# Kernel tuning notes

Hardware: AMD Instinct MI355X
Metric: run time of the kernel (lower is better)

Reference implementation:

```python
import jax, jax.numpy as jnp
import numpy as np

THRESH = 0.2  # contact probability threshold from _make_graph default


def setup_inputs() -> dict:
    key = jax.random.key(0)
    ks = jax.random.split(key, 10)
    L, D, K, M = 1024, 640, 32, 64
    S = jax.random.normal(ks[0], (L, D), jnp.float32)
    P = jax.random.uniform(ks[1], (L, L), jnp.float32)
    P = 0.5 * (P + P.T)  # symmetric base-pair probability matrix
    xyz = jax.random.normal(ks[2], (L, 3), jnp.float32) * 10.0  # Angstrom-scale C1' coords
    rbf_mu = jnp.linspace(0.0, 30.0, K).astype(jnp.float32)     # RBF centers over 0-30 A
    rbf_sigma = jax.random.uniform(ks[3], (K,), jnp.float32, 0.5, 2.0)
    W_edge = jax.random.normal(ks[4], (K + 2, M), jnp.float32) * 0.05
    b_edge = jnp.zeros((M,), jnp.float32)
    W_node = jax.random.normal(ks[5], (D, M), jnp.float32) * 0.05
    w_out = jax.random.normal(ks[6], (M,), jnp.float32) * 0.1
    return {"S": S, "P": P, "xyz": xyz, "rbf_mu": rbf_mu, "rbf_sigma": rbf_sigma,
            "W_edge": W_edge, "b_edge": b_edge, "W_node": W_node, "w_out": w_out}


def reference(S, P, xyz, rbf_mu, rbf_sigma, W_edge, b_edge, W_node, w_out):
    """Graph construction (_make_graph) + one SE3-style gated coordinate update.

    Edges: backbone (j == i+1, etype=0, pij=1) and high-prob contacts
    (P[i,j] > THRESH, j > i+2, etype=1, pij=P[i,j]). Edge scalars are
    [etype, pij, rbf(d)] exactly as in _make_graph; edge vectors are
    xyz[j]-xyz[i]. Computed in dense masked form for jit-compatibility.
    """
    L = xyz.shape[0]
    rel = xyz[None, :, :] - xyz[:, None, :]                      # (L,L,3) xyz[j]-xyz[i]
    # safe norm: eps avoids nan grad on zero diagonal (diagonal is masked out anyway)
    d = jnp.sqrt(jnp.sum(rel * rel, axis=-1, keepdims=True) + 1e-12)  # (L,L,1)
    rbf_feat = jnp.exp(-(d - rbf_mu) ** 2 / (2.0 * rbf_sigma ** 2))   # (L,L,K)

    idx = jnp.arange(L)
    backbone = idx[None, :] == idx[:, None] + 1                  # j == i+1
    contact = (P > THRESH) & (idx[None, :] > idx[:, None] + 2)   # skip j <= i+2
    mask = backbone | contact                                    # (L,L)

    etype = contact.astype(S.dtype)                              # 0 backbone, 1 contact
    pij = jnp.where(backbone, jnp.asarray(1.0, S.dtype), P)
    e_scalar = jnp.concatenate([etype[..., None], pij[..., None], rbf_feat], axis=-1)  # (L,L,K+2)

    # gather-compute: message from edge scalars + destination-node scalars
    node_proj = S @ W_node                                       # (L,M)
    msg = jax.nn.relu(jnp.einsum('ijk,km->ijm', e_scalar, W_edge) + b_edge
                      + node_proj[None, :, :])                   # (L,L,M)
    gate = jax.nn.sigmoid(msg @ w_out) * mask.astype(S.dtype)    # (L,L)

    # scatter: equivariant coordinate update, sum of gated edge vectors per node
    xyz_out = xyz + jnp.einsum('ij,ijc->ic', gate, rel)          # (L,3)
    return xyz_out
```

## Files before the change

kernel.cpp:

```cpp
#include <hip/hip_runtime.h>
#include <math.h>

#define LL 1024
#define DD 640
#define KK 32
#define MM 64
#define THRESH 0.2f

#define NPROJ_OFF 0
#define WRT_OFF   (LL * MM)
#define W0_OFF    (WRT_OFF + 1024)
#define W1_OFF    (W0_OFF + MM)
#define MU_OFF    (W1_OFF + MM)
#define NIS2_OFF  (MU_OFF + KK)

typedef float f32x4_t __attribute__((ext_vector_type(4)));
typedef short bf16x8_t __attribute__((ext_vector_type(8)));

union FragU { unsigned int u[4]; bf16x8_t v; };

__device__ __forceinline__ unsigned int pack_bf(float hi, float lo) {
    return __builtin_amdgcn_perm(__float_as_uint(hi), __float_as_uint(lo), 0x07060302u);
}

__global__ __launch_bounds__(256) void prep_kernel(
    const float* __restrict__ S, const float* __restrict__ rbf_mu,
    const float* __restrict__ rbf_sigma, const float* __restrict__ W_edge,
    const float* __restrict__ b_edge, const float* __restrict__ W_node,
    float* __restrict__ ws)
{
    __shared__ float red[4][2][64];
    const int b = blockIdx.x;
    const int t = threadIdx.x;
    if (b < LL / 2) {
        const int m = t & 63;
        const int c = t >> 6;
        const int r0 = b * 2;
        float a0 = 0.f, a1 = 0.f;
        const int d0 = c * 160;
        #pragma unroll 2
        for (int dd = d0; dd < d0 + 160; dd += 4) {
            const float4 s0 = *(const float4*)(S + (size_t)r0 * DD + dd);
            const float4 s1 = *(const float4*)(S + (size_t)(r0 + 1) * DD + dd);
            const float w0 = W_node[(dd + 0) * MM + m];
            const float w1 = W_node[(dd + 1) * MM + m];
            const float w2 = W_node[(dd + 2) * MM + m];
            const float w3 = W_node[(dd + 3) * MM + m];
            a0 = fmaf(s0.x, w0, a0); a0 = fmaf(s0.y, w1, a0);
            a0 = fmaf(s0.z, w2, a0); a0 = fmaf(s0.w, w3, a0);
            a1 = fmaf(s1.x, w0, a1); a1 = fmaf(s1.y, w1, a1);
            a1 = fmaf(s1.z, w2, a1); a1 = fmaf(s1.w, w3, a1);
        }
        red[c][0][m] = a0;
        red[c][1][m] = a1;
        __syncthreads();
        if (t < 64) {
            const float be = b_edge[t];
            const float v0 = ((red[0][0][t] + red[1][0][t]) + (red[2][0][t] + red[3][0][t])) + be;
            const float v1 = ((red[0][1][t] + red[1][1][t]) + (red[2][1][t] + red[3][1][t])) + be;
            ws[NPROJ_OFF + (size_t)r0 * MM + t]       = v0;
            ws[NPROJ_OFF + (size_t)(r0 + 1) * MM + t] = v1;
        }
    } else {
        unsigned short* wrt = (unsigned short*)(ws + WRT_OFF);
        if (t < MM) {
            ws[W0_OFF + t] = W_edge[t];
            ws[W1_OFF + t] = W_edge[MM + t];
        }
        if (t < KK) {
            ws[MU_OFF + t] = rbf_mu[t];
            const float s = rbf_sigma[t];
            ws[NIS2_OFF + t] = -1.0f / (2.0f * s * s);
        }
        for (int idx = t; idx < KK * MM; idx += 256) {
            const int m = idx >> 5, k = idx & 31;
            unsigned int u = __float_as_uint(W_edge[(2 + k) * MM + m]);
            u = (u + 0x7fffu + ((u >> 16) & 1u)) >> 16;
            wrt[idx] = (unsigned short)u;
        }
    }
}

__global__ __launch_bounds__(256, 2) void edge_kernel(
    const float* __restrict__ P, const float* __restrict__ xyz,
    const float* __restrict__ w_out, const float* __restrict__ ws,
    float* __restrict__ out)
{
    const int tid  = threadIdx.x;
    const int lane = tid & 63;
    const int wave = tid >> 6;
    const int quad = lane >> 4;
    const int col  = lane & 15;
    __shared__ float sred[4][3];

    const float* __restrict__ nproj = ws + NPROJ_OFF;
    const unsigned short* __restrict__ wrt = (const unsigned short*)(ws + WRT_OFF);

    FragU ar[4], a2[4];
    float wv[4][4];
    float muj[8], nis2[8];
    #pragma unroll
    for (int mt = 0; mt < 4; ++mt) {
        const uint4 w = *(const uint4*)(wrt + (mt * 16 + col) * KK + quad * 8);
        ar[mt].u[0] = w.x; ar[mt].u[1] = w.y; ar[mt].u[2] = w.z; ar[mt].u[3] = w.w;
        const float w0 = ws[W0_OFF + mt * 16 + col];
        const float w1 = ws[W1_OFF + mt * 16 + col];
        a2[mt].u[0] = (quad == 0) ? pack_bf(w1, w0) : 0u;
        a2[mt].u[1] = 0u; a2[mt].u[2] = 0u; a2[mt].u[3] = 0u;
        const float4 wo = *(const float4*)(w_out + mt * 16 + quad * 4);
        wv[mt][0] = wo.x; wv[mt][1] = wo.y; wv[mt][2] = wo.z; wv[mt][3] = wo.w;
    }
    #pragma unroll
    for (int j = 0; j < 8; ++j) {
        muj[j]  = ws[MU_OFF + quad * 8 + j];
        nis2[j] = ws[NIS2_OFF + quad * 8 + j];
    }

    int rows[2];
    rows[0] = (int)blockIdx.x;
    rows[1] = (LL - 1) - (int)blockIdx.x;

    for (int rr = 0; rr < 2; ++rr) {
        const int i = rows[rr];
        const float xi0 = xyz[i * 3 + 0];
        const float xi1 = xyz[i * 3 + 1];
        const float xi2 = xyz[i * 3 + 2];
        float ax = 0.f, ay = 0.f, az = 0.f;
        const int len = (LL - 1) - i;

        for (int base = wave * 64; base < len; base += 256) {
            const int jo = base + lane;
            const bool valid = jo < len;
            const int jc = valid ? (i + 1 + jo) : (LL - 1);
            const float p_own = P[(size_t)i * LL + jc];
            const float rx = xyz[jc * 3 + 0] - xi0;
            const float ry = xyz[jc * 3 + 1] - xi1;
            const float rz = xyz[jc * 3 + 2] - xi2;
            const float d_own = sqrtf(fmaf(rx, rx, fmaf(ry, ry, fmaf(rz, rz, 1e-12f))));
            const bool msk = valid && ((jo == 0) || ((jo >= 2) && (p_own > THRESH)));

            float res[4];
            #pragma unroll
            for (int ct = 0; ct < 4; ++ct) {
                const int src = ct * 16 + col;
                const float d_t = __shfl(d_own, src, 64);
                const float p_t = __shfl(p_own, src, 64);
                const int jo_t = base + src;
                const float et = ((jo_t >= 2) && (p_t > THRESH)) ? 1.0f : 0.0f;
                const float pj = (jo_t == 0) ? 1.0f : p_t;

                float r[8];
                #pragma unroll
                for (int j = 0; j < 8; ++j) {
                    const float t0 = d_t - muj[j];
                    r[j] = __expf(t0 * t0 * nis2[j]);
                }
                FragU bf;
                bf.u[0] = pack_bf(r[1], r[0]); bf.u[1] = pack_bf(r[3], r[2]);
                bf.u[2] = pack_bf(r[5], r[4]); bf.u[3] = pack_bf(r[7], r[6]);
                FragU b2;
                b2.u[0] = (quad == 0) ? pack_bf(pj, et) : 0u;
                b2.u[1] = 0u; b2.u[2] = 0u; b2.u[3] = 0u;

                const int jc_t = (jo_t < len) ? (i + 1 + jo_t) : (LL - 1);
                const float* npr = nproj + (size_t)jc_t * MM;

                float g = 0.0f;
                #pragma unroll
                for (int mt = 0; mt < 4; ++mt) {
                    f32x4_t c0 = *(const f32x4_t*)(npr + mt * 16 + quad * 4);
                    c0 = __builtin_amdgcn_mfma_f32_16x16x32_bf16(ar[mt].v, bf.v, c0, 0, 0, 0);
                    c0 = __builtin_amdgcn_mfma_f32_16x16x32_bf16(a2[mt].v, b2.v, c0, 0, 0, 0);
                    g = fmaf(fmaxf(c0[0], 0.f), wv[mt][0], g);
                    g = fmaf(fmaxf(c0[1], 0.f), wv[mt][1], g);
                    g = fmaf(fmaxf(c0[2], 0.f), wv[mt][2], g);
                    g = fmaf(fmaxf(c0[3], 0.f), wv[mt][3], g);
                }
                g += __shfl_xor(g, 16, 64);
                g += __shfl_xor(g, 32, 64);
                res[ct] = g;
            }
            float gd = res[0];
            gd = (quad == 1) ? res[1] : gd;
            gd = (quad == 2) ? res[2] : gd;
            gd = (quad == 3) ? res[3] : gd;
            const float gate = msk ? (1.0f / (1.0f + __expf(-gd))) : 0.0f;
            ax = fmaf(gate, rx, ax);
            ay = fmaf(gate, ry, ay);
            az = fmaf(gate, rz, az);
        }

        #pragma unroll
        for (int off = 32; off > 0; off >>= 1) {
            ax += __shfl_down(ax, off, 64);
            ay += __shfl_down(ay, off, 64);
            az += __shfl_down(az, off, 64);
        }
        if (lane == 0) {
            sred[wave][0] = ax; sred[wave][1] = ay; sred[wave][2] = az;
        }
        __syncthreads();
        if (tid == 0) {
            const float tx = (sred[0][0] + sred[1][0]) + (sred[2][0] + sred[3][0]);
            const float ty = (sred[0][1] + sred[1][1]) + (sred[2][1] + sred[3][1]);
            const float tz = (sred[0][2] + sred[1][2]) + (sred[2][2] + sred[3][2]);
            out[i * 3 + 0] = xi0 + tx;
            out[i * 3 + 1] = xi1 + ty;
            out[i * 3 + 2] = xi2 + tz;
        }
        __syncthreads();
    }
}

extern "C" void kernel_launch(void* const* d_in, const int* in_sizes, int n_in,
                              void* d_out, int out_size, void* d_ws, size_t ws_size,
                              hipStream_t stream) {
    const float* S         = (const float*)d_in[0];
    const float* P         = (const float*)d_in[1];
    const float* xyz       = (const float*)d_in[2];
    const float* rbf_mu    = (const float*)d_in[3];
    const float* rbf_sigma = (const float*)d_in[4];
    const float* W_edge    = (const float*)d_in[5];
    const float* b_edge    = (const float*)d_in[6];
    const float* W_node    = (const float*)d_in[7];
    const float* w_out     = (const float*)d_in[8];
    float* out = (float*)d_out;
    float* ws  = (float*)d_ws;

    prep_kernel<<<LL / 2 + 1, 256, 0, stream>>>(S, rbf_mu, rbf_sigma, W_edge,
                                                b_edge, W_node, ws);
    edge_kernel<<<LL / 2, 256, 0, stream>>>(P, xyz, w_out, ws, out);
}
```

Measured before the change: 104.2 us.

## Drop second MFMA for etype/pij, recompute per-column distances, widen edge blocks

Replaces the second bf16 MFMA that added the etype/pij edge-scalar contribution with two fp32 FMAs per accumulator element, folded into the node-projection accumulator before the main MFMA. Instead of shuffling distance and P across lanes, each lane reloads P and xyz for its column and recomputes the distance directly. The edge kernel now runs 512-thread blocks (8 waves) with launch bounds (512,4), and the prep loop unroll rises to 4. These aim to cut MFMA count and shuffle traffic and to raise parallelism per row, at the cost of redundant global loads and sqrt work and more register pressure under the tighter launch bound.

```diff
diff --git a/kernel.cpp b/kernel.cpp
--- a/kernel.cpp
+++ b/kernel.cpp
@@ -38,7 +38,7 @@
         const int r0 = b * 2;
         float a0 = 0.f, a1 = 0.f;
         const int d0 = c * 160;
-        #pragma unroll 2
+        #pragma unroll 4
         for (int dd = d0; dd < d0 + 160; dd += 4) {
             const float4 s0 = *(const float4*)(S + (size_t)r0 * DD + dd);
             const float4 s1 = *(const float4*)(S + (size_t)(r0 + 1) * DD + dd);
@@ -81,7 +81,7 @@
     }
 }
 
-__global__ __launch_bounds__(256, 2) void edge_kernel(
+__global__ __launch_bounds__(512, 4) void edge_kernel(
     const float* __restrict__ P, const float* __restrict__ xyz,
     const float* __restrict__ w_out, const float* __restrict__ ws,
     float* __restrict__ out)
@@ -91,24 +91,21 @@
     const int wave = tid >> 6;
     const int quad = lane >> 4;
     const int col  = lane & 15;
-    __shared__ float sred[4][3];
+    __shared__ float sred[8][3];
 
     const float* __restrict__ nproj = ws + NPROJ_OFF;
     const unsigned short* __restrict__ wrt = (const unsigned short*)(ws + WRT_OFF);
 
-    FragU ar[4], a2[4];
-    float wv[4][4];
+    FragU ar[4];
+    f32x4_t w0q[4], w1q[4], wv[4];
     float muj[8], nis2[8];
     #pragma unroll
     for (int mt = 0; mt < 4; ++mt) {
         const uint4 w = *(const uint4*)(wrt + (mt * 16 + col) * KK + quad * 8);
         ar[mt].u[0] = w.x; ar[mt].u[1] = w.y; ar[mt].u[2] = w.z; ar[mt].u[3] = w.w;
-        const float w0 = ws[W0_OFF + mt * 16 + col];
-        const float w1 = ws[W1_OFF + mt * 16 + col];
-        a2[mt].u[0] = (quad == 0) ? pack_bf(w1, w0) : 0u;
-        a2[mt].u[1] = 0u; a2[mt].u[2] = 0u; a2[mt].u[3] = 0u;
-        const float4 wo = *(const float4*)(w_out + mt * 16 + quad * 4);
-        wv[mt][0] = wo.x; wv[mt][1] = wo.y; wv[mt][2] = wo.z; wv[mt][3] = wo.w;
+        w0q[mt] = *(const f32x4_t*)(ws + W0_OFF + mt * 16 + quad * 4);
+        w1q[mt] = *(const f32x4_t*)(ws + W1_OFF + mt * 16 + quad * 4);
+        wv[mt]  = *(const f32x4_t*)(w_out + mt * 16 + quad * 4);
     }
     #pragma unroll
     for (int j = 0; j < 8; ++j) {
@@ -128,7 +125,7 @@
         float ax = 0.f, ay = 0.f, az = 0.f;
         const int len = (LL - 1) - i;
 
-        for (int base = wave * 64; base < len; base += 256) {
+        for (int base = wave * 64; base < len; base += 512) {
             const int jo = base + lane;
             const bool valid = jo < len;
             const int jc = valid ? (i + 1 + jo) : (LL - 1);
@@ -136,41 +133,41 @@
             const float rx = xyz[jc * 3 + 0] - xi0;
             const float ry = xyz[jc * 3 + 1] - xi1;
             const float rz = xyz[jc * 3 + 2] - xi2;
-            const float d_own = sqrtf(fmaf(rx, rx, fmaf(ry, ry, fmaf(rz, rz, 1e-12f))));
             const bool msk = valid && ((jo == 0) || ((jo >= 2) && (p_own > THRESH)));
 
             float res[4];
             #pragma unroll
             for (int ct = 0; ct < 4; ++ct) {
-                const int src = ct * 16 + col;
-                const float d_t = __shfl(d_own, src, 64);
-                const float p_t = __shfl(p_own, src, 64);
-                const int jo_t = base + src;
-                const float et = ((jo_t >= 2) && (p_t > THRESH)) ? 1.0f : 0.0f;
-                const float pj = (jo_t == 0) ? 1.0f : p_t;
+                const int jo_n = base + ct * 16 + col;
+                const int jc_n = (jo_n < len) ? (i + 1 + jo_n) : (LL - 1);
+                const float p_n = P[(size_t)i * LL + jc_n];
+                const float dx = xyz[jc_n * 3 + 0] - xi0;
+                const float dy = xyz[jc_n * 3 + 1] - xi1;
+                const float dz = xyz[jc_n * 3 + 2] - xi2;
+                const float d_n = sqrtf(fmaf(dx, dx, fmaf(dy, dy, fmaf(dz, dz, 1e-12f))));
+                const float et = ((jo_n >= 2) && (p_n > THRESH)) ? 1.0f : 0.0f;
+                const float pj = (jo_n == 0) ? 1.0f : p_n;
 
                 float r[8];
                 #pragma unroll
                 for (int j = 0; j < 8; ++j) {
-                    const float t0 = d_t - muj[j];
+                    const float t0 = d_n - muj[j];
                     r[j] = __expf(t0 * t0 * nis2[j]);
                 }
                 FragU bf;
                 bf.u[0] = pack_bf(r[1], r[0]); bf.u[1] = pack_bf(r[3], r[2]);
                 bf.u[2] = pack_bf(r[5], r[4]); bf.u[3] = pack_bf(r[7], r[6]);
-                FragU b2;
-                b2.u[0] = (quad == 0) ? pack_bf(pj, et) : 0u;
-                b2.u[1] = 0u; b2.u[2] = 0u; b2.u[3] = 0u;
-
-                const int jc_t = (jo_t < len) ? (i + 1 + jo_t) : (LL - 1);
-                const float* npr = nproj + (size_t)jc_t * MM;
-
+
+                const float* npr = nproj + (size_t)jc_n * MM;
                 float g = 0.0f;
                 #pragma unroll
                 for (int mt = 0; mt < 4; ++mt) {
                     f32x4_t c0 = *(const f32x4_t*)(npr + mt * 16 + quad * 4);
+                    c0[0] = fmaf(et, w0q[mt][0], fmaf(pj, w1q[mt][0], c0[0]));
+                    c0[1] = fmaf(et, w0q[mt][1], fmaf(pj, w1q[mt][1], c0[1]));
+                    c0[2] = fmaf(et, w0q[mt][2], fmaf(pj, w1q[mt][2], c0[2]));
+                    c0[3] = fmaf(et, w0q[mt][3], fmaf(pj, w1q[mt][3], c0[3]));
                     c0 = __builtin_amdgcn_mfma_f32_16x16x32_bf16(ar[mt].v, bf.v, c0, 0, 0, 0);
-                    c0 = __builtin_amdgcn_mfma_f32_16x16x32_bf16(a2[mt].v, b2.v, c0, 0, 0, 0);
                     g = fmaf(fmaxf(c0[0], 0.f), wv[mt][0], g);
                     g = fmaf(fmaxf(c0[1], 0.f), wv[mt][1], g);
                     g = fmaf(fmaxf(c0[2], 0.f), wv[mt][2], g);
@@ -201,9 +198,11 @@
         }
         __syncthreads();
         if (tid == 0) {
-            const float tx = (sred[0][0] + sred[1][0]) + (sred[2][0] + sred[3][0]);
-            const float ty = (sred[0][1] + sred[1][1]) + (sred[2][1] + sred[3][1]);
-            const float tz = (sred[0][2] + sred[1][2]) + (sred[2][2] + sred[3][2]);
+            float tx = 0.f, ty = 0.f, tz = 0.f;
+            #pragma unroll
+            for (int w = 0; w < 8; ++w) {
+                tx += sred[w][0]; ty += sred[w][1]; tz += sred[w][2];
+            }
             out[i * 3 + 0] = xi0 + tx;
             out[i * 3 + 1] = xi1 + ty;
             out[i * 3 + 2] = xi2 + tz;
@@ -229,5 +228,5 @@
 
     prep_kernel<<<LL / 2 + 1, 256, 0, stream>>>(S, rbf_mu, rbf_sigma, W_edge,
                                                 b_edge, W_node, ws);
-    edge_kernel<<<LL / 2, 256, 0, stream>>>(P, xyz, w_out, ws, out);
-}
+    edge_kernel<<<LL / 2, 512, 0, stream>>>(P, xyz, w_out, ws, out);
+}
```

Measured after the change: 102.5 us. No clear change (-1.6%).
